# Kernel optimization log

Hardware: AMD Instinct MI355X
Metric: run time of the kernel (lower is better)

## Reference

```python
import jax, jax.numpy as jnp
import numpy as np

B, A, C, H, W = 16, 5, 512, 16, 16


def _affine_grid(theta, Hh, Ww):
    # torch F.affine_grid, align_corners=False (default). theta: [2,3]
    xs = (2.0 * jnp.arange(Ww, dtype=jnp.float32) + 1.0) / Ww - 1.0  # [W]
    ys = (2.0 * jnp.arange(Hh, dtype=jnp.float32) + 1.0) / Hh - 1.0  # [H]
    gx = theta[0, 0] * xs[None, :] + theta[0, 1] * ys[:, None] + theta[0, 2]  # [H,W]
    gy = theta[1, 0] * xs[None, :] + theta[1, 1] * ys[:, None] + theta[1, 2]  # [H,W]
    return gx, gy


def _grid_sample(img, gx, gy):
    # torch F.grid_sample, bilinear, padding_mode='zeros', align_corners=False
    # img: [C,H,W]; gx,gy: [H,W] normalized coords
    C_, Hh, Ww = img.shape
    ix = ((gx + 1.0) * Ww - 1.0) * 0.5
    iy = ((gy + 1.0) * Hh - 1.0) * 0.5
    x0 = jnp.floor(ix); y0 = jnp.floor(iy)
    x1 = x0 + 1.0;      y1 = y0 + 1.0
    wx1 = ix - x0; wx0 = 1.0 - wx1
    wy1 = iy - y0; wy0 = 1.0 - wy1

    def gather(xi, yi):
        inb = (xi >= 0) & (xi < Ww) & (yi >= 0) & (yi < Hh)
        xc = jnp.clip(xi, 0, Ww - 1).astype(jnp.int32)
        yc = jnp.clip(yi, 0, Hh - 1).astype(jnp.int32)
        return img[:, yc, xc] * inb[None].astype(img.dtype)  # [C,H,W]

    return (gather(x0, y0) * (wx0 * wy0)[None] + gather(x1, y0) * (wx1 * wy0)[None]
          + gather(x0, y1) * (wx0 * wy1)[None] + gather(x1, y1) * (wx1 * wy1)[None])


def _warp(nb_feat, nb_warp):
    # nb_feat: [C,H,W] neighbor feature; nb_warp: [4,4] pose matrix
    zero = jnp.zeros((), dtype=jnp.float32)
    one = jnp.ones((), dtype=jnp.float32)
    theta_rot = jnp.stack([
        jnp.stack([nb_warp[0, 0], nb_warp[0, 1], zero]),
        jnp.stack([nb_warp[1, 0], nb_warp[1, 1], zero])])  # [2,3]
    gx_r, gy_r = _affine_grid(theta_rot, H, W)
    feat_rot = _grid_sample(nb_feat, gx_r, gy_r)
    x_trans = 4.0 * nb_warp[0, 3] / 128.0
    y_trans = -(4.0 * nb_warp[1, 3]) / 128.0
    theta_trans = jnp.stack([
        jnp.stack([one, zero, x_trans]),
        jnp.stack([zero, one, y_trans])])
    gx_t, gy_t = _affine_grid(theta_trans, H, W)
    return _grid_sample(feat_rot, gx_t, gy_t)  # [C,H,W]


def _fuse_one(local_b, trans_b, n):
    # local_b: [A,C,H,W], trans_b: [A,A,4,4], n: scalar num_agent
    # pair[i,j] = warp of agent j's feature into agent i's frame
    pair = jax.vmap(lambda t_i: jax.vmap(_warp)(local_b, t_i))(trans_b)  # [A,A,C,H,W]
    idx = jnp.arange(A)
    mask = (idx[:, None] != idx[None, :]) & (idx[:, None] < n) & (idx[None, :] < n)
    return local_b + jnp.einsum('ij,ijchw->ichw', mask.astype(local_b.dtype), pair)


def setup_inputs() -> dict:
    key = jax.random.key(0)
    k1, k2, k3, k4 = jax.random.split(key, 4)
    feat_maps = jax.random.normal(k1, (A * B, C, H, W), dtype=jnp.float32)
    # realistic near-rigid pose matrices: rotation block + translation column
    ang = jax.random.uniform(k2, (B, A, A), minval=-0.5, maxval=0.5)
    tr = jax.random.normal(k3, (B, A, A, 2), dtype=jnp.float32) * 8.0
    tm = jnp.zeros((B, A, A, 4, 4), dtype=jnp.float32)
    tm = tm.at[..., 0, 0].set(jnp.cos(ang)).at[..., 0, 1].set(-jnp.sin(ang))
    tm = tm.at[..., 1, 0].set(jnp.sin(ang)).at[..., 1, 1].set(jnp.cos(ang))
    tm = tm.at[..., 0, 3].set(tr[..., 0]).at[..., 1, 3].set(tr[..., 1])
    tm = tm.at[..., 2, 2].set(1.0).at[..., 3, 3].set(1.0)
    num_agent = jax.random.randint(k4, (B, A), 1, 6, dtype=jnp.int64) if jax.config.jax_enable_x64 else jax.random.randint(k4, (B, A), 1, 6, dtype=jnp.int32)
    return {"feat_maps": feat_maps, "trans_matrices": tm, "num_agent_tensor": num_agent}


def reference(feat_maps, trans_matrices, num_agent_tensor):
    # feat_maps is agent-major blocks of size B (feat_maps[B*i:B*(i+1)] is agent i)
    local = feat_maps.reshape(A, B, C, H, W).transpose(1, 0, 2, 3, 4)  # [B,A,C,H,W]
    fused = jax.vmap(_fuse_one)(local, trans_matrices, num_agent_tensor[:, 0])
    # agents2batch: concat agents along batch dim -> [A*B,C,H,W]
    return fused.transpose(1, 0, 2, 3, 4).reshape(A * B, C, H, W)
```

## Files before the change

kernel.cpp:

```cpp
#include <hip/hip_runtime.h>

#define NB 16
#define NA 5
#define NC 512
#define HW 256
#define NBLK 2560
#define NITEM 2

typedef float f4 __attribute__((ext_vector_type(4)));
typedef _Float16 h8 __attribute__((ext_vector_type(8)));

static __device__ __forceinline__ h8 splat8(float v) {
    const _Float16 h = (_Float16)v;
    h8 r = {h, h, h, h, h, h, h, h};
    return r;
}

static __device__ __forceinline__ h8 rot_sample(const h8* __restrict__ src,
                                                float ixr, float iyr, float ws) {
    const float fx0 = floorf(ixr), fy0 = floorf(iyr);
    const float wx1 = ixr - fx0,   wy1 = iyr - fy0;
    const int ix0 = (int)fx0, iy0 = (int)fy0;
    const int ix1 = ix0 + 1,  iy1 = iy0 + 1;
    const float mx0 = (ix0 >= 0 && ix0 < 16) ? (1.0f - wx1) : 0.0f;
    const float mx1 = (ix1 >= 0 && ix1 < 16) ? wx1 : 0.0f;
    const float my0 = (iy0 >= 0 && iy0 < 16) ? (1.0f - wy1) * ws : 0.0f;
    const float my1 = (iy1 >= 0 && iy1 < 16) ? wy1 * ws : 0.0f;
    const int cx0 = min(max(ix0, 0), 15), cx1 = min(max(ix1, 0), 15);
    const int cy0 = min(max(iy0, 0), 15), cy1 = min(max(iy1, 0), 15);
    const h8 v00 = src[cy0 * 16 + cx0];
    const h8 v01 = src[cy0 * 16 + cx1];
    const h8 v10 = src[cy1 * 16 + cx0];
    const h8 v11 = src[cy1 * 16 + cx1];
    const h8 hx0 = splat8(mx0), hx1 = splat8(mx1);
    const h8 hy0 = splat8(my0), hy1 = splat8(my1);
    return (v00 * hx0 + v01 * hx1) * hy0 + (v10 * hx0 + v11 * hx1) * hy1;
}

__global__ __launch_bounds__(256) void fafmimo_persist_kernel(
    const float* __restrict__ feat,
    const float* __restrict__ trans,
    const int*   __restrict__ numa,
    float*       __restrict__ out)
{
    __shared__ h8 lds_nb[4][HW];

    const int p = threadIdx.x;
    const int x = p & 15, y = p >> 4;
    bool lds_dirty = false;

#pragma unroll
    for (int it = 0; it < NITEM; ++it) {
        const int item = blockIdx.x + it * NBLK;
        const int g  = item & 63;
        const int r  = item >> 6;
        const int i  = r % NA;
        const int b  = r / NA;
        const int c0 = g << 3;
        const int n  = numa[b * NA];
        const bool work = (i < n) && (n > 1);

        const float* own = feat + ((i * NB + b) * NC + c0) * HW + p;
        float acc[8];
#pragma unroll
        for (int k = 0; k < 8; ++k) acc[k] = own[k * HW];

        if (work) {
            if (lds_dirty) __syncthreads();
            f4 r0v[4], r1v[4];
#pragma unroll
            for (int jj = 0; jj < 4; ++jj) {
                const int j = jj + (jj >= i);
                if (j < n) {
                    const f4* tw = (const f4*)(trans + (((b * NA) + i) * NA + j) * 16);
                    r0v[jj] = tw[0];
                    r1v[jj] = tw[1];
                    const float* src = feat + ((j * NB + b) * NC + c0) * HW + p;
                    h8 v;
#pragma unroll
                    for (int k = 0; k < 8; ++k) v[k] = (_Float16)src[k * HW];
                    lds_nb[jj][p] = v;
                }
            }
            __syncthreads();
            lds_dirty = true;

            h8 pair_acc = splat8(0.0f);
#pragma unroll
            for (int jj = 0; jj < 4; ++jj) {
                const int j = jj + (jj >= i);
                if (j < n) {
                    const float r00 = r0v[jj].x, r01 = r0v[jj].y;
                    const float r10 = r1v[jj].x, r11 = r1v[jj].y;

                    const float dx = 0.25f * r0v[jj].w;
                    const float dy = -0.25f * r1v[jj].w;
                    const float fdx = floorf(dx), fdy = floorf(dy);
                    const float tx1 = dx - fdx, tx0 = 1.0f - tx1;
                    const float ty1 = dy - fdy, ty0 = 1.0f - ty1;
                    const int ox = x + (int)fdx;
                    const int oy = y + (int)fdy;
                    const bool inx0 = (ox >= 0) && (ox < 16);
                    const bool inx1 = (ox + 1 >= 0) && (ox + 1 < 16);
                    const bool iny0 = (oy >= 0) && (oy < 16);
                    const bool iny1 = (oy + 1 >= 0) && (oy + 1 < 16);
                    const float ws00 = (inx0 && iny0) ? tx0 * ty0 : 0.0f;
                    const float ws10 = (inx1 && iny0) ? tx1 * ty0 : 0.0f;
                    const float ws01 = (inx0 && iny1) ? tx0 * ty1 : 0.0f;
                    const float ws11 = (inx1 && iny1) ? tx1 * ty1 : 0.0f;

                    const float fox = (float)ox - 7.5f;
                    const float foy = (float)oy - 7.5f;
                    const float bxr = r00 * fox + r01 * foy + 7.5f;
                    const float byr = r10 * fox + r11 * foy + 7.5f;

                    const h8* srcj = &lds_nb[jj][0];
                    pair_acc += rot_sample(srcj, bxr,             byr,             ws00);
                    pair_acc += rot_sample(srcj, bxr + r00,       byr + r10,       ws10);
                    pair_acc += rot_sample(srcj, bxr + r01,       byr + r11,       ws01);
                    pair_acc += rot_sample(srcj, bxr + r00 + r01, byr + r10 + r11, ws11);
                }
            }
#pragma unroll
            for (int k = 0; k < 8; ++k) acc[k] += (float)pair_acc[k];
        }

        float* dst = out + ((i * NB + b) * NC + c0) * HW + p;
#pragma unroll
        for (int k = 0; k < 8; ++k) dst[k * HW] = acc[k];
    }
}

extern "C" void kernel_launch(void* const* d_in, const int* in_sizes, int n_in,
                              void* d_out, int out_size, void* d_ws, size_t ws_size,
                              hipStream_t stream) {
    const float* feat  = (const float*)d_in[0];
    const float* trans = (const float*)d_in[1];
    const int*   numa  = (const int*)d_in[2];
    float* out = (float*)d_out;

    fafmimo_persist_kernel<<<dim3(NBLK), dim3(256), 0, stream>>>(
        feat, trans, numa, out);
}
```

Before: 102.8 us.

## Software-pipeline persistent kernel: prefetch next item's features while computing current

Result: faster. 99.93 us (-2.8%).

```diff
diff --git a/kernel.cpp b/kernel.cpp
--- a/kernel.cpp
+++ b/kernel.cpp
@@ -4,8 +4,8 @@
 #define NA 5
 #define NC 512
 #define HW 256
-#define NBLK 2560
-#define NITEM 2
+#define NBLK 2048
+#define NTOT 5120
 
 typedef float f4 __attribute__((ext_vector_type(4)));
 typedef _Float16 h8 __attribute__((ext_vector_type(8)));
@@ -16,28 +16,81 @@
     return r;
 }
 
-static __device__ __forceinline__ h8 rot_sample(const h8* __restrict__ src,
-                                                float ixr, float iyr, float ws) {
-    const float fx0 = floorf(ixr), fy0 = floorf(iyr);
-    const float wx1 = ixr - fx0,   wy1 = iyr - fy0;
-    const int ix0 = (int)fx0, iy0 = (int)fy0;
-    const int ix1 = ix0 + 1,  iy1 = iy0 + 1;
-    const float mx0 = (ix0 >= 0 && ix0 < 16) ? (1.0f - wx1) : 0.0f;
-    const float mx1 = (ix1 >= 0 && ix1 < 16) ? wx1 : 0.0f;
-    const float my0 = (iy0 >= 0 && iy0 < 16) ? (1.0f - wy1) * ws : 0.0f;
-    const float my1 = (iy1 >= 0 && iy1 < 16) ? wy1 * ws : 0.0f;
-    const int cx0 = min(max(ix0, 0), 15), cx1 = min(max(ix1, 0), 15);
-    const int cy0 = min(max(iy0, 0), 15), cy1 = min(max(iy1, 0), 15);
-    const h8 v00 = src[cy0 * 16 + cx0];
-    const h8 v01 = src[cy0 * 16 + cx1];
-    const h8 v10 = src[cy1 * 16 + cx0];
-    const h8 v11 = src[cy1 * 16 + cx1];
-    const h8 hx0 = splat8(mx0), hx1 = splat8(mx1);
-    const h8 hy0 = splat8(my0), hy1 = splat8(my1);
-    return (v00 * hx0 + v01 * hx1) * hy0 + (v10 * hx0 + v11 * hx1) * hy1;
+static __device__ __forceinline__ h8 rot_sample2(const h8* __restrict__ src,
+        float xA, float yA, float wA,
+        float xB, float yB, float wB) {
+    const float fxA = floorf(xA), fyA = floorf(yA);
+    const float fxB = floorf(xB), fyB = floorf(yB);
+    const int ixA = (int)fxA, iyA = (int)fyA;
+    const int ixB = (int)fxB, iyB = (int)fyB;
+    const float wxA1 = xA - fxA, wyA1 = yA - fyA;
+    const float wxB1 = xB - fxB, wyB1 = yB - fyB;
+    const float mxA0 = (ixA     >= 0 && ixA     < 16) ? 1.0f - wxA1 : 0.0f;
+    const float mxA1 = (ixA + 1 >= 0 && ixA + 1 < 16) ? wxA1 : 0.0f;
+    const float myA0 = (iyA     >= 0 && iyA     < 16) ? (1.0f - wyA1) * wA : 0.0f;
+    const float myA1 = (iyA + 1 >= 0 && iyA + 1 < 16) ? wyA1 * wA : 0.0f;
+    const float mxB0 = (ixB     >= 0 && ixB     < 16) ? 1.0f - wxB1 : 0.0f;
+    const float mxB1 = (ixB + 1 >= 0 && ixB + 1 < 16) ? wxB1 : 0.0f;
+    const float myB0 = (iyB     >= 0 && iyB     < 16) ? (1.0f - wyB1) * wB : 0.0f;
+    const float myB1 = (iyB + 1 >= 0 && iyB + 1 < 16) ? wyB1 * wB : 0.0f;
+    const int cxA0 = min(max(ixA, 0), 15), cxA1 = min(max(ixA + 1, 0), 15);
+    const int cyA0 = min(max(iyA, 0), 15), cyA1 = min(max(iyA + 1, 0), 15);
+    const int cxB0 = min(max(ixB, 0), 15), cxB1 = min(max(ixB + 1, 0), 15);
+    const int cyB0 = min(max(iyB, 0), 15), cyB1 = min(max(iyB + 1, 0), 15);
+    const h8 vA00 = src[cyA0 * 16 + cxA0];
+    const h8 vA01 = src[cyA0 * 16 + cxA1];
+    const h8 vA10 = src[cyA1 * 16 + cxA0];
+    const h8 vA11 = src[cyA1 * 16 + cxA1];
+    const h8 vB00 = src[cyB0 * 16 + cxB0];
+    const h8 vB01 = src[cyB0 * 16 + cxB1];
+    const h8 vB10 = src[cyB1 * 16 + cxB0];
+    const h8 vB11 = src[cyB1 * 16 + cxB1];
+    return (vA00 * splat8(mxA0) + vA01 * splat8(mxA1)) * splat8(myA0)
+         + (vA10 * splat8(mxA0) + vA11 * splat8(mxA1)) * splat8(myA1)
+         + (vB00 * splat8(mxB0) + vB01 * splat8(mxB1)) * splat8(myB0)
+         + (vB10 * splat8(mxB0) + vB11 * splat8(mxB1)) * splat8(myB1);
 }
 
-__global__ __launch_bounds__(256) void fafmimo_persist_kernel(
+struct Item {
+    int i, b, c0, n;
+    bool work;
+    float own[8];
+    float nb[4][8];
+    f4 r0[4], r1[4];
+};
+
+static __device__ __forceinline__ Item prefetch_item(
+        const float* __restrict__ feat, const float* __restrict__ trans,
+        const int* __restrict__ numa, int idx, int p) {
+    Item it;
+    const int g = idx & 63;
+    const int r = idx >> 6;
+    it.i = r % NA;
+    it.b = r / NA;
+    it.c0 = g << 3;
+    it.n = numa[it.b * NA];
+    it.work = (it.i < it.n) && (it.n > 1);
+    const float* own = feat + ((it.i * NB + it.b) * NC + it.c0) * HW + p;
+#pragma unroll
+    for (int k = 0; k < 8; ++k) it.own[k] = own[k * HW];
+    if (it.work) {
+#pragma unroll
+        for (int jj = 0; jj < 4; ++jj) {
+            const int j = jj + (jj >= it.i);
+            if (j < it.n) {
+                const f4* tw = (const f4*)(trans + (((it.b * NA) + it.i) * NA + j) * 16);
+                it.r0[jj] = tw[0];
+                it.r1[jj] = tw[1];
+                const float* src = feat + ((j * NB + it.b) * NC + it.c0) * HW + p;
+#pragma unroll
+                for (int k = 0; k < 8; ++k) it.nb[jj][k] = src[k * HW];
+            }
+        }
+    }
+    return it;
+}
+
+__global__ __launch_bounds__(256) void fafmimo_pipe_kernel(
     const float* __restrict__ feat,
     const float* __restrict__ trans,
     const int*   __restrict__ numa,
@@ -47,54 +100,48 @@
 
     const int p = threadIdx.x;
     const int x = p & 15, y = p >> 4;
-    bool lds_dirty = false;
+    bool dirty = false;
 
-#pragma unroll
-    for (int it = 0; it < NITEM; ++it) {
-        const int item = blockIdx.x + it * NBLK;
-        const int g  = item & 63;
-        const int r  = item >> 6;
-        const int i  = r % NA;
-        const int b  = r / NA;
-        const int c0 = g << 3;
-        const int n  = numa[b * NA];
-        const bool work = (i < n) && (n > 1);
+    int idx = blockIdx.x;
+    Item cur = prefetch_item(feat, trans, numa, idx, p);
 
-        const float* own = feat + ((i * NB + b) * NC + c0) * HW + p;
-        float acc[8];
-#pragma unroll
-        for (int k = 0; k < 8; ++k) acc[k] = own[k * HW];
-
-        if (work) {
-            if (lds_dirty) __syncthreads();
-            f4 r0v[4], r1v[4];
+    while (true) {
+        if (cur.work) {
+            if (dirty) __syncthreads();
 #pragma unroll
             for (int jj = 0; jj < 4; ++jj) {
-                const int j = jj + (jj >= i);
-                if (j < n) {
-                    const f4* tw = (const f4*)(trans + (((b * NA) + i) * NA + j) * 16);
-                    r0v[jj] = tw[0];
-                    r1v[jj] = tw[1];
-                    const float* src = feat + ((j * NB + b) * NC + c0) * HW + p;
+                const int j = jj + (jj >= cur.i);
+                if (j < cur.n) {
                     h8 v;
 #pragma unroll
-                    for (int k = 0; k < 8; ++k) v[k] = (_Float16)src[k * HW];
+                    for (int k = 0; k < 8; ++k) v[k] = (_Float16)cur.nb[jj][k];
                     lds_nb[jj][p] = v;
                 }
             }
             __syncthreads();
-            lds_dirty = true;
+            dirty = true;
+        }
 
+        const int nidx = idx + NBLK;
+        const bool more = nidx < NTOT;
+        Item nxt;
+        if (more) nxt = prefetch_item(feat, trans, numa, nidx, p);
+
+        float acc[8];
+#pragma unroll
+        for (int k = 0; k < 8; ++k) acc[k] = cur.own[k];
+
+        if (cur.work) {
             h8 pair_acc = splat8(0.0f);
 #pragma unroll
             for (int jj = 0; jj < 4; ++jj) {
-                const int j = jj + (jj >= i);
-                if (j < n) {
-                    const float r00 = r0v[jj].x, r01 = r0v[jj].y;
-                    const float r10 = r1v[jj].x, r11 = r1v[jj].y;
+                const int j = jj + (jj >= cur.i);
+                if (j < cur.n) {
+                    const float r00 = cur.r0[jj].x, r01 = cur.r0[jj].y;
+                    const float r10 = cur.r1[jj].x, r11 = cur.r1[jj].y;
 
-                    const float dx = 0.25f * r0v[jj].w;
-                    const float dy = -0.25f * r1v[jj].w;
+                    const float dx = 0.25f * cur.r0[jj].w;
+                    const float dy = -0.25f * cur.r1[jj].w;
                     const float fdx = floorf(dx), fdy = floorf(dy);
                     const float tx1 = dx - fdx, tx0 = 1.0f - tx1;
                     const float ty1 = dy - fdy, ty0 = 1.0f - ty1;
@@ -115,19 +162,25 @@
                     const float byr = r10 * fox + r11 * foy + 7.5f;
 
                     const h8* srcj = &lds_nb[jj][0];
-                    pair_acc += rot_sample(srcj, bxr,             byr,             ws00);
-                    pair_acc += rot_sample(srcj, bxr + r00,       byr + r10,       ws10);
-                    pair_acc += rot_sample(srcj, bxr + r01,       byr + r11,       ws01);
-                    pair_acc += rot_sample(srcj, bxr + r00 + r01, byr + r10 + r11, ws11);
+                    pair_acc += rot_sample2(srcj,
+                        bxr,       byr,       ws00,
+                        bxr + r00, byr + r10, ws10);
+                    pair_acc += rot_sample2(srcj,
+                        bxr + r01,       byr + r11,       ws01,
+                        bxr + r00 + r01, byr + r10 + r11, ws11);
                 }
             }
 #pragma unroll
             for (int k = 0; k < 8; ++k) acc[k] += (float)pair_acc[k];
         }
 
-        float* dst = out + ((i * NB + b) * NC + c0) * HW + p;
+        float* dst = out + ((cur.i * NB + cur.b) * NC + cur.c0) * HW + p;
 #pragma unroll
         for (int k = 0; k < 8; ++k) dst[k * HW] = acc[k];
+
+        if (!more) break;
+        cur = nxt;
+        idx = nidx;
     }
 }
 
@@ -139,6 +192,6 @@
     const int*   numa  = (const int*)d_in[2];
     float* out = (float*)d_out;
 
-    fafmimo_persist_kernel<<<dim3(NBLK), dim3(256), 0, stream>>>(
+    fafmimo_pipe_kernel<<<dim3(NBLK), dim3(256), 0, stream>>>(
         feat, trans, numa, out);
 }
```

## Split warp into two passes per wave with LDS intermediate and float4 I/O

Applied to the files above, without the earlier changes.

Result: no change. 102.3 us (-0.4%).

```diff
diff --git a/kernel.cpp b/kernel.cpp
--- a/kernel.cpp
+++ b/kernel.cpp
@@ -4,130 +4,149 @@
 #define NA 5
 #define NC 512
 #define HW 256
-#define NBLK 2560
-#define NITEM 2
+#define NGQ 128
+#define NTOT (NA * NB * NGQ)
+#define NBLK 1024
+#define NWAVES (NBLK * 4)
 
 typedef float f4 __attribute__((ext_vector_type(4)));
-typedef _Float16 h8 __attribute__((ext_vector_type(8)));
+typedef _Float16 h4 __attribute__((ext_vector_type(4)));
 
-static __device__ __forceinline__ h8 splat8(float v) {
+static __device__ __forceinline__ h4 splat4h(float v) {
     const _Float16 h = (_Float16)v;
-    h8 r = {h, h, h, h, h, h, h, h};
+    h4 r = {h, h, h, h};
     return r;
 }
 
-static __device__ __forceinline__ h8 rot_sample(const h8* __restrict__ src,
-                                                float ixr, float iyr, float ws) {
-    const float fx0 = floorf(ixr), fy0 = floorf(iyr);
-    const float wx1 = ixr - fx0,   wy1 = iyr - fy0;
-    const int ix0 = (int)fx0, iy0 = (int)fy0;
-    const int ix1 = ix0 + 1,  iy1 = iy0 + 1;
-    const float mx0 = (ix0 >= 0 && ix0 < 16) ? (1.0f - wx1) : 0.0f;
-    const float mx1 = (ix1 >= 0 && ix1 < 16) ? wx1 : 0.0f;
-    const float my0 = (iy0 >= 0 && iy0 < 16) ? (1.0f - wy1) * ws : 0.0f;
-    const float my1 = (iy1 >= 0 && iy1 < 16) ? wy1 * ws : 0.0f;
-    const int cx0 = min(max(ix0, 0), 15), cx1 = min(max(ix1, 0), 15);
-    const int cy0 = min(max(iy0, 0), 15), cy1 = min(max(iy1, 0), 15);
-    const h8 v00 = src[cy0 * 16 + cx0];
-    const h8 v01 = src[cy0 * 16 + cx1];
-    const h8 v10 = src[cy1 * 16 + cx0];
-    const h8 v11 = src[cy1 * 16 + cx1];
-    const h8 hx0 = splat8(mx0), hx1 = splat8(mx1);
-    const h8 hy0 = splat8(my0), hy1 = splat8(my1);
-    return (v00 * hx0 + v01 * hx1) * hy0 + (v10 * hx0 + v11 * hx1) * hy1;
-}
-
-__global__ __launch_bounds__(256) void fafmimo_persist_kernel(
+__global__ __launch_bounds__(256) void fafmimo_wave_kernel(
     const float* __restrict__ feat,
     const float* __restrict__ trans,
     const int*   __restrict__ numa,
     float*       __restrict__ out)
 {
-    __shared__ h8 lds_nb[4][HW];
+    __shared__ h4 lds_slab[4][4][HW];
+    __shared__ h4 lds_fr[4][HW];
 
-    const int p = threadIdx.x;
-    const int x = p & 15, y = p >> 4;
-    bool lds_dirty = false;
+    const int w    = threadIdx.x >> 6;
+    const int lane = threadIdx.x & 63;
+    const int px0  = lane << 2;
+    const int qy   = px0 >> 4;
+    const int qx   = px0 & 15;
+    const float fy = (float)qy - 7.5f;
 
-#pragma unroll
-    for (int it = 0; it < NITEM; ++it) {
-        const int item = blockIdx.x + it * NBLK;
-        const int g  = item & 63;
-        const int r  = item >> 6;
+    h4* const slab_w = &lds_slab[w][0][0];
+    h4* const fr_w   = &lds_fr[w][0];
+    const int wgid = blockIdx.x * 4 + w;
+
+    for (int it = 0; it < 3; ++it) {
+        const int idx = wgid + it * NWAVES;
+        if (idx >= NTOT) break;
+        const int g  = idx & (NGQ - 1);
+        const int r  = idx >> 7;
         const int i  = r % NA;
         const int b  = r / NA;
-        const int c0 = g << 3;
+        const int c0 = g << 2;
         const int n  = numa[b * NA];
         const bool work = (i < n) && (n > 1);
 
-        const float* own = feat + ((i * NB + b) * NC + c0) * HW + p;
-        float acc[8];
+        const float* own = feat + (size_t)((i * NB + b) * NC + c0) * HW + px0;
+        f4 acc[4];
 #pragma unroll
-        for (int k = 0; k < 8; ++k) acc[k] = own[k * HW];
+        for (int k = 0; k < 4; ++k) acc[k] = *(const f4*)(own + k * HW);
 
         if (work) {
-            if (lds_dirty) __syncthreads();
-            f4 r0v[4], r1v[4];
 #pragma unroll
             for (int jj = 0; jj < 4; ++jj) {
                 const int j = jj + (jj >= i);
                 if (j < n) {
-                    const f4* tw = (const f4*)(trans + (((b * NA) + i) * NA + j) * 16);
-                    r0v[jj] = tw[0];
-                    r1v[jj] = tw[1];
-                    const float* src = feat + ((j * NB + b) * NC + c0) * HW + p;
-                    h8 v;
+                    const float* src = feat + (size_t)((j * NB + b) * NC + c0) * HW + px0;
+                    f4 v[4];
 #pragma unroll
-                    for (int k = 0; k < 8; ++k) v[k] = (_Float16)src[k * HW];
-                    lds_nb[jj][p] = v;
+                    for (int k = 0; k < 4; ++k) v[k] = *(const f4*)(src + k * HW);
+#pragma unroll
+                    for (int q = 0; q < 4; ++q) {
+                        h4 hv = { (_Float16)v[0][q], (_Float16)v[1][q],
+                                  (_Float16)v[2][q], (_Float16)v[3][q] };
+                        slab_w[jj * HW + px0 + q] = hv;
+                    }
                 }
             }
-            __syncthreads();
-            lds_dirty = true;
+            __builtin_amdgcn_wave_barrier();
 
-            h8 pair_acc = splat8(0.0f);
+            h4 pair_acc[4] = {splat4h(0.f), splat4h(0.f), splat4h(0.f), splat4h(0.f)};
+
 #pragma unroll
             for (int jj = 0; jj < 4; ++jj) {
                 const int j = jj + (jj >= i);
                 if (j < n) {
-                    const float r00 = r0v[jj].x, r01 = r0v[jj].y;
-                    const float r10 = r1v[jj].x, r11 = r1v[jj].y;
+                    const float* tb = trans + (size_t)(((b * NA) + i) * NA + j) * 16;
+                    const f4 row0 = *(const f4*)tb;
+                    const f4 row1 = *(const f4*)(tb + 4);
+                    const float r00 = row0.x, r01 = row0.y;
+                    const float r10 = row1.x, r11 = row1.y;
+                    const h4* sj = slab_w + jj * HW;
 
-                    const float dx = 0.25f * r0v[jj].w;
-                    const float dy = -0.25f * r1v[jj].w;
+#pragma unroll
+                    for (int q = 0; q < 4; ++q) {
+                        const float fx = (float)(qx + q) - 7.5f;
+                        const float ixr = r00 * fx + r01 * fy + 7.5f;
+                        const float iyr = r10 * fx + r11 * fy + 7.5f;
+                        const float fx0 = floorf(ixr), fy0 = floorf(iyr);
+                        const float wx1 = ixr - fx0, wy1 = iyr - fy0;
+                        const int ix0 = (int)fx0, iy0 = (int)fy0;
+                        const float mx0 = (ix0 >= 0 && ix0 < 16) ? 1.f - wx1 : 0.f;
+                        const float mx1 = (ix0 + 1 >= 0 && ix0 + 1 < 16) ? wx1 : 0.f;
+                        const float my0 = (iy0 >= 0 && iy0 < 16) ? 1.f - wy1 : 0.f;
+                        const float my1 = (iy0 + 1 >= 0 && iy0 + 1 < 16) ? wy1 : 0.f;
+                        const int cx0 = min(max(ix0, 0), 15), cx1 = min(max(ix0 + 1, 0), 15);
+                        const int cy0 = min(max(iy0, 0), 15), cy1 = min(max(iy0 + 1, 0), 15);
+                        const h4 v00 = sj[cy0 * 16 + cx0], v01 = sj[cy0 * 16 + cx1];
+                        const h4 v10 = sj[cy1 * 16 + cx0], v11 = sj[cy1 * 16 + cx1];
+                        const h4 frq = (v00 * splat4h(mx0) + v01 * splat4h(mx1)) * splat4h(my0)
+                                     + (v10 * splat4h(mx0) + v11 * splat4h(mx1)) * splat4h(my1);
+                        fr_w[px0 + q] = frq;
+                    }
+                    __builtin_amdgcn_wave_barrier();
+
+                    const float dx = 0.25f * row0.w;
+                    const float dy = -0.25f * row1.w;
                     const float fdx = floorf(dx), fdy = floorf(dy);
-                    const float tx1 = dx - fdx, tx0 = 1.0f - tx1;
-                    const float ty1 = dy - fdy, ty0 = 1.0f - ty1;
-                    const int ox = x + (int)fdx;
-                    const int oy = y + (int)fdy;
-                    const bool inx0 = (ox >= 0) && (ox < 16);
-                    const bool inx1 = (ox + 1 >= 0) && (ox + 1 < 16);
+                    const float tx1 = dx - fdx, tx0 = 1.f - tx1;
+                    const float ty1 = dy - fdy, ty0 = 1.f - ty1;
+                    const int sdx = (int)fdx, sdy = (int)fdy;
+                    const int oy = qy + sdy;
                     const bool iny0 = (oy >= 0) && (oy < 16);
                     const bool iny1 = (oy + 1 >= 0) && (oy + 1 < 16);
-                    const float ws00 = (inx0 && iny0) ? tx0 * ty0 : 0.0f;
-                    const float ws10 = (inx1 && iny0) ? tx1 * ty0 : 0.0f;
-                    const float ws01 = (inx0 && iny1) ? tx0 * ty1 : 0.0f;
-                    const float ws11 = (inx1 && iny1) ? tx1 * ty1 : 0.0f;
-
-                    const float fox = (float)ox - 7.5f;
-                    const float foy = (float)oy - 7.5f;
-                    const float bxr = r00 * fox + r01 * foy + 7.5f;
-                    const float byr = r10 * fox + r11 * foy + 7.5f;
-
-                    const h8* srcj = &lds_nb[jj][0];
-                    pair_acc += rot_sample(srcj, bxr,             byr,             ws00);
-                    pair_acc += rot_sample(srcj, bxr + r00,       byr + r10,       ws10);
-                    pair_acc += rot_sample(srcj, bxr + r01,       byr + r11,       ws01);
-                    pair_acc += rot_sample(srcj, bxr + r00 + r01, byr + r10 + r11, ws11);
+                    const float wya = iny0 ? ty0 : 0.f;
+                    const float wyb = iny1 ? ty1 : 0.f;
+                    const int cya = min(max(oy, 0), 15), cyb = min(max(oy + 1, 0), 15);
+#pragma unroll
+                    for (int q = 0; q < 4; ++q) {
+                        const int ox = qx + q + sdx;
+                        const bool inx0 = (ox >= 0) && (ox < 16);
+                        const bool inx1 = (ox + 1 >= 0) && (ox + 1 < 16);
+                        const float wxa = inx0 ? tx0 : 0.f;
+                        const float wxb = inx1 ? tx1 : 0.f;
+                        const int cxa = min(max(ox, 0), 15), cxb = min(max(ox + 1, 0), 15);
+                        const h4 t00 = fr_w[cya * 16 + cxa], t01 = fr_w[cya * 16 + cxb];
+                        const h4 t10 = fr_w[cyb * 16 + cxa], t11 = fr_w[cyb * 16 + cxb];
+                        pair_acc[q] += (t00 * splat4h(wxa) + t01 * splat4h(wxb)) * splat4h(wya)
+                                     + (t10 * splat4h(wxa) + t11 * splat4h(wxb)) * splat4h(wyb);
+                    }
+                    __builtin_amdgcn_wave_barrier();
                 }
             }
 #pragma unroll
-            for (int k = 0; k < 8; ++k) acc[k] += (float)pair_acc[k];
+            for (int q = 0; q < 4; ++q)
+#pragma unroll
+                for (int k = 0; k < 4; ++k)
+                    acc[k][q] += (float)pair_acc[q][k];
         }
 
-        float* dst = out + ((i * NB + b) * NC + c0) * HW + p;
+        float* dst = out + (size_t)((i * NB + b) * NC + c0) * HW + px0;
 #pragma unroll
-        for (int k = 0; k < 8; ++k) dst[k * HW] = acc[k];
+        for (int k = 0; k < 4; ++k) *(f4*)(dst + k * HW) = acc[k];
+        __builtin_amdgcn_wave_barrier();
     }
 }
 
@@ -139,6 +158,6 @@
     const int*   numa  = (const int*)d_in[2];
     float* out = (float*)d_out;
 
-    fafmimo_persist_kernel<<<dim3(NBLK), dim3(256), 0, stream>>>(
+    fafmimo_wave_kernel<<<dim3(NBLK), dim3(256), 0, stream>>>(
         feat, trans, numa, out);
 }
```
